# Performance work log

Hardware: AMD Instinct MI355X
Metric: run time of the kernel (lower is better)

The kernel has to match this reference:

```python
import jax, jax.numpy as jnp
import numpy as np

OBS_DIM = 512
ACT_DIM = 32
HIDDEN_DIM = 1024
MSG_DIM = 128
POS_EM_DIM = 128
T = 256


def pos_table(n, dim):
    pos = np.arange(n)[:, None].astype(np.float64)
    j = np.arange(dim)[None, :]
    tab = pos / np.power(10000.0, 2 * (j // 2) / dim)
    tab[:, 0::2] = np.sin(tab[:, 0::2])
    tab[:, 1::2] = np.cos(tab[:, 1::2])
    return tab.astype(np.float32)


def setup_inputs() -> dict:
    key = jax.random.key(0)
    ks = jax.random.split(key, 12)
    in_dim = 1 + ACT_DIM
    s = 0.1
    return {
        "obs": jax.random.normal(ks[0], (T, OBS_DIM), jnp.float32),
        "prev_act": jax.random.normal(ks[1], (T, ACT_DIM), jnp.float32),
        "in_shift": jnp.zeros((OBS_DIM,), jnp.float32),
        "in_scale": jnp.ones((OBS_DIM,), jnp.float32),
        "pos_embedding": jnp.asarray(pos_table(HIDDEN_DIM, POS_EM_DIM)),
        "W_ih": s * jax.random.normal(ks[2], (4 * POS_EM_DIM, in_dim), jnp.float32),
        "b_ih": s * jax.random.normal(ks[3], (4 * POS_EM_DIM,), jnp.float32),
        "W_hh": s * jax.random.normal(ks[4], (4 * POS_EM_DIM, POS_EM_DIM), jnp.float32),
        "b_hh": s * jax.random.normal(ks[5], (4 * POS_EM_DIM,), jnp.float32),
        "Wq": s * jax.random.normal(ks[6], (MSG_DIM, POS_EM_DIM), jnp.float32),
        "bq": s * jax.random.normal(ks[7], (MSG_DIM,), jnp.float32),
        "Wk": s * jax.random.normal(ks[8], (MSG_DIM, POS_EM_DIM), jnp.float32),
        "bk": s * jax.random.normal(ks[9], (MSG_DIM,), jnp.float32),
    }


def reference(obs, prev_act, in_shift, in_scale, pos_embedding,
              W_ih, b_ih, W_hh, b_hh, Wq, bq, Wk, bk):
    # input normalization (buffers default to identity)
    x = (obs - in_shift) / (in_scale + 1e-8)  # (T, obs_dim)
    # query projection of the positional table is constant across steps
    q = pos_embedding @ Wq.T + bq             # (hidden_dim, msg_dim)
    inv_scale = 1.0 / jnp.sqrt(jnp.float32(MSG_DIM))

    def step(carry, inp):
        h, c = carry                            # (obs_dim, pos_em_dim) each
        s, a = inp                              # (obs_dim,), (act_dim,)
        # state-action pair: each obs scalar paired with the full prev action
        xa = jnp.concatenate(
            [s[:, None], jnp.broadcast_to(a, (OBS_DIM, ACT_DIM))], axis=-1)
        gates = xa @ W_ih.T + b_ih + h @ W_hh.T + b_hh
        i, f, g, o = jnp.split(gates, 4, axis=-1)  # torch LSTMCell gate order
        c = jax.nn.sigmoid(f) * c + jax.nn.sigmoid(i) * jnp.tanh(g)
        h = jax.nn.sigmoid(o) * jnp.tanh(c)
        k = h @ Wk.T + bk                       # (obs_dim, msg_dim)
        w = jnp.tanh((q @ k.T) * inv_scale)     # (hidden_dim, obs_dim)
        out = w @ s                             # (hidden_dim,)
        return (h, c), out

    h0 = jnp.zeros((OBS_DIM, POS_EM_DIM), x.dtype)
    c0 = jnp.zeros_like(h0)
    _, outs = jax.lax.scan(step, (h0, c0), (x, prev_act))
    return jnp.tanh(outs)                       # (T, hidden_dim)
```

## Files before the change

kernel.cpp:

```cpp
#include <hip/hip_runtime.h>
#include <hip/hip_fp16.h>

#define T_STEPS 256
#define OBS 512
#define ACT 32
#define HID 1024
#define PED 128
#define MSG 128
#define GATES 512
#define HSTR 136
#define KSTR 17
#define L1 1.4426950408889634f
#define L2C 2.8853900817779268f
#define QSCALE 0.2550348805576823f

typedef _Float16 half8  __attribute__((ext_vector_type(8)));
typedef float    floatx4 __attribute__((ext_vector_type(4)));

__device__ __forceinline__ float fast_exp2(float x) { return __builtin_amdgcn_exp2f(x); }
__device__ __forceinline__ float fast_rcp(float x)  { return __builtin_amdgcn_rcpf(x); }
__device__ __forceinline__ float tanh_f(float x) {
    return fmaf(-2.0f, fast_rcp(fast_exp2(2.8853900817779268f * x) + 1.0f), 1.0f);
}

__global__ void k_pre(const float* __restrict__ obs, const float* __restrict__ act,
                      const float* __restrict__ shift, const float* __restrict__ scale,
                      const float* __restrict__ W_ih, const float* __restrict__ b_ih,
                      const float* __restrict__ b_hh,
                      float* __restrict__ xnorm, float* __restrict__ apre_p) {
    int t = blockIdx.x;
    int tid = threadIdx.x;
    __shared__ float a_s[ACT];
    if (tid < ACT) a_s[tid] = act[t * ACT + tid];
    __syncthreads();
    for (int n = tid; n < OBS; n += 256) {
        xnorm[t * OBS + n] = (obs[t * OBS + n] - shift[n]) / (scale[n] + 1e-8f);
    }
    for (int j = tid; j < GATES; j += 256) {
        float acc = b_ih[j] + b_hh[j];
        const float* wr = W_ih + j * 33 + 1;
#pragma unroll
        for (int u = 0; u < ACT; ++u) acc = fmaf(a_s[u], wr[u], acc);
        int g = j >> 7, p = j & 127;
        apre_p[t * GATES + p * 4 + g] = acc;
    }
}

__global__ void k_qproj(const float* __restrict__ pe, const float* __restrict__ Wq,
                        const float* __restrict__ bq, const float* __restrict__ Wk,
                        const float* __restrict__ bk,
                        _Float16* __restrict__ qh, float* __restrict__ cb) {
    int m = blockIdx.x;
    int d = threadIdx.x;
    __shared__ float pe_s[PED];
    __shared__ float q_s[PED];
    __shared__ float red_s[2];
    pe_s[d] = pe[m * PED + d];
    __syncthreads();
    const float* wr = Wq + d * PED;
    float a = bq[d];
#pragma unroll 8
    for (int p = 0; p < PED; ++p) a = fmaf(pe_s[p], wr[p], a);
    q_s[d] = a;
    float pb = a * bk[d];
#pragma unroll
    for (int off = 32; off; off >>= 1) pb += __shfl_xor(pb, off, 64);
    if ((d & 63) == 0) red_s[d >> 6] = pb;
    __syncthreads();
    float acc = 0.f;
#pragma unroll 8
    for (int p = 0; p < PED; ++p) acc = fmaf(q_s[p], Wk[p * PED + d], acc);
    qh[m * PED + d] = (_Float16)(acc * QSCALE);
    if (d == 0) cb[m] = (red_s[0] + red_s[1]) * QSCALE;
}

__global__ __launch_bounds__(512, 1)
void k_lstm(const float* __restrict__ xnorm, const float* __restrict__ apre_p,
            const float* __restrict__ W_ih, const float* __restrict__ W_hh,
            _Float16* __restrict__ H16) {
    const int tid = threadIdx.x;
    const int lane = tid & 63, wv = tid >> 6;
    const int l15 = lane & 15, quad = lane >> 4;
    const int n0 = blockIdx.x * 8;
    const int p = 16 * wv + l15;
    const int base = (quad & 1) * 4 + ((quad >> 1) * 2);

    half8 bfr[4][4];
    float wih0[4];
#pragma unroll
    for (int g = 0; g < 4; ++g) {
        const int col = 128 * g + p;
        const float* wrow = W_hh + (size_t)col * PED;
#pragma unroll
        for (int c = 0; c < 4; ++c) {
            const int k0 = c * 32 + quad * 8;
            float4 f0 = *(const float4*)(wrow + k0);
            float4 f1 = *(const float4*)(wrow + k0 + 4);
            bfr[g][c] = (half8){(_Float16)f0.x, (_Float16)f0.y, (_Float16)f0.z, (_Float16)f0.w,
                                (_Float16)f1.x, (_Float16)f1.y, (_Float16)f1.z, (_Float16)f1.w};
        }
        wih0[g] = W_ih[(size_t)col * 33];
    }

    __shared__ _Float16 h_s[2][16 * HSTR];
    __shared__ float x_s[T_STEPS * 8];

    for (int idx = tid; idx < T_STEPS * 8; idx += 512)
        x_s[idx] = xnorm[(idx >> 3) * OBS + n0 + (idx & 7)];
    for (int idx = tid; idx < 2 * 16 * HSTR; idx += 512)
        ((_Float16*)h_s)[idx] = (_Float16)0.f;

    float c0 = 0.f, c1 = 0.f;
    const float* apl = apre_p + p * 4;
    float4 ap = *(const float4*)(apl);
    __syncthreads();

    int buf = 0;
    for (int t = 0; t < T_STEPS; ++t) {
        half8 af[4];
        const _Float16* hb = h_s[buf] + l15 * HSTR + quad * 8;
#pragma unroll
        for (int c = 0; c < 4; ++c) af[c] = *(const half8*)(hb + c * 32);

        floatx4 acc[4];
#pragma unroll
        for (int g = 0; g < 4; ++g) {
            acc[g] = (floatx4){0.f, 0.f, 0.f, 0.f};
#pragma unroll
            for (int c = 0; c < 4; ++c)
                acc[g] = __builtin_amdgcn_mfma_f32_16x16x32_f16(
                    af[c], bfr[g][c], acc[g], 0, 0, 0);
        }

        const int tn = (t + 1 < T_STEPS) ? t + 1 : t;
        float4 ap_n = *(const float4*)(apl + tn * GATES);

        float gA[4], gB[4];
#pragma unroll
        for (int g = 0; g < 4; ++g) {
            float s2 = __shfl_xor(acc[g][2], 32, 64);
            float s3 = __shfl_xor(acc[g][3], 32, 64);
            gA[g] = (quad < 2) ? acc[g][0] : s2;
            gB[g] = (quad < 2) ? acc[g][1] : s3;
        }

        const float xA = x_s[t * 8 + base];
        const float xB = x_s[t * 8 + base + 1];
        float gi0 = fmaf(xA, wih0[0], gA[0] + ap.x);
        float gf0 = fmaf(xA, wih0[1], gA[1] + ap.y);
        float gg0 = fmaf(xA, wih0[2], gA[2] + ap.z);
        float go0 = fmaf(xA, wih0[3], gA[3] + ap.w);
        float gi1 = fmaf(xB, wih0[0], gB[0] + ap.x);
        float gf1 = fmaf(xB, wih0[1], gB[1] + ap.y);
        float gg1 = fmaf(xB, wih0[2], gB[2] + ap.z);
        float go1 = fmaf(xB, wih0[3], gB[3] + ap.w);

        float Di0 = 1.f + fast_exp2(fminf(-L1 * gi0, 20.f));
        float Df0 = 1.f + fast_exp2(fminf(-L1 * gf0, 20.f));
        float Dg0 = 1.f + fast_exp2(fminf(L2C * gg0, 20.f));
        float Di1 = 1.f + fast_exp2(fminf(-L1 * gi1, 20.f));
        float Df1 = 1.f + fast_exp2(fminf(-L1 * gf1, 20.f));
        float Dg1 = 1.f + fast_exp2(fminf(L2C * gg1, 20.f));
        float t0 = Df0 * Dg0, C0 = Di0 * t0;
        float t1 = Df1 * Dg1, C1 = Di1 * t1;
        float rp = fast_rcp(C0 * C1);
        float rA = rp * C1, rB = rp * C0;
        float iDi0 = rA * t0, iDf0 = rA * (Di0 * Dg0), iDg0 = rA * (Di0 * Df0);
        float iDi1 = rB * t1, iDf1 = rB * (Di1 * Dg1), iDg1 = rB * (Di1 * Df1);
        float cn0 = fmaf(iDf0, c0, iDi0 * fmaf(-2.f, iDg0, 1.f));
        float cn1 = fmaf(iDf1, c1, iDi1 * fmaf(-2.f, iDg1, 1.f));
        c0 = cn0; c1 = cn1;
        float Do0 = 1.f + fast_exp2(fminf(-L1 * go0, 20.f));
        float Do1 = 1.f + fast_exp2(fminf(-L1 * go1, 20.f));
        float Dc0 = 1.f + fast_exp2(fminf(L2C * cn0, 20.f));
        float Dc1 = 1.f + fast_exp2(fminf(L2C * cn1, 20.f));
        float m0 = Do0 * Dc0, m1 = Do1 * Dc1;
        float rq = fast_rcp(m0 * m1);
        float qA = rq * m1, qB = rq * m0;
        float iDo0 = qA * Dc0, iDc0 = qA * Do0;
        float iDo1 = qB * Dc1, iDc1 = qB * Do1;
        _Float16 hA = (_Float16)(iDo0 * fmaf(-2.f, iDc0, 1.f));
        _Float16 hB = (_Float16)(iDo1 * fmaf(-2.f, iDc1, 1.f));

        _Float16* hn = h_s[buf ^ 1];
        hn[base * HSTR + p] = hA;
        hn[(base + 1) * HSTR + p] = hB;
        _Float16* Hg = H16 + (size_t)t * (OBS * MSG) + (size_t)(n0 + base) * MSG + p;
        Hg[0] = hA;
        Hg[MSG] = hB;

        ap = ap_n;
        buf ^= 1;
        __syncthreads();
    }
}

__global__ __launch_bounds__(256, 4)
void k_attn(const _Float16* __restrict__ qh, const float* __restrict__ cb,
            const _Float16* __restrict__ H16, const float* __restrict__ xnorm,
            float* __restrict__ outp) {
    const int t = blockIdx.x >> 3;
    const int mq = blockIdx.x & 7;
    const int tid = threadIdx.x;
    const int lane = tid & 63, wave = tid >> 6;
    const int l15 = lane & 15, quad = lane >> 4;
    const int m0 = mq * 128 + wave * 32;

    half8 afrag[2][4];
    floatx4 cbv[2];
#pragma unroll
    for (int mt = 0; mt < 2; ++mt) {
        const half8* qrow = (const half8*)(qh + (size_t)(m0 + mt * 16 + l15) * PED);
#pragma unroll
        for (int c = 0; c < 4; ++c) afrag[mt][c] = qrow[c * 4 + quad];
        cbv[mt] = *(const floatx4*)(cb + m0 + mt * 16 + quad * 4);
    }

    __shared__ half8 kbuf[64 * KSTR];
    __shared__ float s_s[64];

    float outacc[8];
#pragma unroll
    for (int i = 0; i < 8; ++i) outacc[i] = 0.f;

    const half8* Ht = (const half8*)(H16 + (size_t)t * (OBS * MSG));
    half8 pf[4];
    float sf = 0.f;
#pragma unroll
    for (int i = 0; i < 4; ++i) pf[i] = Ht[i * 256 + tid];
    if (tid < 64) sf = xnorm[t * OBS + tid];

    for (int ch = 0; ch < 8; ++ch) {
        __syncthreads();
#pragma unroll
        for (int i = 0; i < 4; ++i) {
            int f = i * 256 + tid;
            kbuf[(f >> 4) * KSTR + (f & 15)] = pf[i];
        }
        if (tid < 64) s_s[tid] = sf;
        __syncthreads();
        if (ch < 7) {
            const half8* Hn = Ht + (ch + 1) * 1024;
#pragma unroll
            for (int i = 0; i < 4; ++i) pf[i] = Hn[i * 256 + tid];
            if (tid < 64) sf = xnorm[t * OBS + (ch + 1) * 64 + tid];
        }

#pragma unroll
        for (int nt = 0; nt < 4; ++nt) {
            half8 bfrag[4];
#pragma unroll
            for (int c = 0; c < 4; ++c)
                bfrag[c] = kbuf[(nt * 16 + l15) * KSTR + c * 4 + quad];

            floatx4 acc[2];
#pragma unroll
            for (int mt = 0; mt < 2; ++mt) {
                acc[mt] = cbv[mt];
#pragma unroll
                for (int c = 0; c < 4; ++c)
                    acc[mt] = __builtin_amdgcn_mfma_f32_16x16x32_f16(
                        afrag[mt][c], bfrag[c], acc[mt], 0, 0, 0);
            }

            const float sv = s_s[nt * 16 + l15];
#pragma unroll
            for (int mt = 0; mt < 2; ++mt) {
                float E0 = fast_exp2(fminf(acc[mt][0], 20.f));
                float E1 = fast_exp2(fminf(acc[mt][1], 20.f));
                float E2 = fast_exp2(fminf(acc[mt][2], 20.f));
                float E3 = fast_exp2(fminf(acc[mt][3], 20.f));
                float D0 = 1.f + E0, D1 = 1.f + E1, D2 = 1.f + E2, D3 = 1.f + E3;
                float m01 = D0 * D1, m23 = D2 * D3;
                float rp = fast_rcp(m01 * m23);
                float rA = rp * m23, rB = rp * m01;
                float i0 = rA * D1, i1 = rA * D0, i2 = rB * D3, i3 = rB * D2;
                outacc[mt * 4 + 0] = fmaf(fmaf(-2.f, i0, 1.f), sv, outacc[mt * 4 + 0]);
                outacc[mt * 4 + 1] = fmaf(fmaf(-2.f, i1, 1.f), sv, outacc[mt * 4 + 1]);
                outacc[mt * 4 + 2] = fmaf(fmaf(-2.f, i2, 1.f), sv, outacc[mt * 4 + 2]);
                outacc[mt * 4 + 3] = fmaf(fmaf(-2.f, i3, 1.f), sv, outacc[mt * 4 + 3]);
            }
        }
    }

#pragma unroll
    for (int i = 0; i < 8; ++i) {
        float v = outacc[i];
        v += __shfl_xor(v, 1, 16);
        v += __shfl_xor(v, 2, 16);
        v += __shfl_xor(v, 4, 16);
        v += __shfl_xor(v, 8, 16);
        outacc[i] = v;
    }
    if (l15 == 0) {
        const int mbase = m0 + quad * 4;
#pragma unroll
        for (int mt = 0; mt < 2; ++mt)
#pragma unroll
            for (int r = 0; r < 4; ++r)
                outp[(size_t)t * HID + mbase + mt * 16 + r] = tanh_f(outacc[mt * 4 + r]);
    }
}

extern "C" void kernel_launch(void* const* d_in, const int* in_sizes, int n_in,
                              void* d_out, int out_size, void* d_ws, size_t ws_size,
                              hipStream_t stream) {
    const float* obs      = (const float*)d_in[0];
    const float* prev_act = (const float*)d_in[1];
    const float* in_shift = (const float*)d_in[2];
    const float* in_scale = (const float*)d_in[3];
    const float* pos_emb  = (const float*)d_in[4];
    const float* W_ih     = (const float*)d_in[5];
    const float* b_ih     = (const float*)d_in[6];
    const float* W_hh     = (const float*)d_in[7];
    const float* b_hh     = (const float*)d_in[8];
    const float* Wq       = (const float*)d_in[9];
    const float* bq       = (const float*)d_in[10];
    const float* Wk       = (const float*)d_in[11];
    const float* bk       = (const float*)d_in[12];
    float* outp = (float*)d_out;

    float* ws = (float*)d_ws;
    float* xnorm  = ws;
    float* apre_p = ws + 131072;
    _Float16* qh  = (_Float16*)(ws + 262144);
    float* cbuf   = ws + 327680;
    _Float16* H16 = (_Float16*)(ws + 328704);

    k_pre<<<T_STEPS, 256, 0, stream>>>(obs, prev_act, in_shift, in_scale,
                                       W_ih, b_ih, b_hh, xnorm, apre_p);
    k_qproj<<<HID, 128, 0, stream>>>(pos_emb, Wq, bq, Wk, bk, qh, cbuf);
    k_lstm<<<64, 512, 0, stream>>>(xnorm, apre_p, W_ih, W_hh, H16);
    k_attn<<<T_STEPS * 8, 256, 0, stream>>>(qh, cbuf, H16, xnorm, outp);
}
```

Before: 335.2 us.

## Halve LSTM rows per block, seed MFMA with bias, stream attention K directly

The LSTM kernel now handles 4 obs rows per block instead of 8 and launches 128 blocks. This spreads the serial recurrence over more CUs and removes the cross-lane shuffles and the two-row gate math, while leaving more MFMA rows padded. The gate bias is loaded into the MFMA accumulator as its starting value. The attention kernel drops its LDS staging and barriers and loads H fragments from global memory into registers with a one-tile prefetch, trading shared-memory reuse for fewer syncs.

```diff
diff --git a/kernel.cpp b/kernel.cpp
--- a/kernel.cpp
+++ b/kernel.cpp
@@ -9,7 +9,6 @@
 #define MSG 128
 #define GATES 512
 #define HSTR 136
-#define KSTR 17
 #define L1 1.4426950408889634f
 #define L2C 2.8853900817779268f
 #define QSCALE 0.2550348805576823f
@@ -81,9 +80,8 @@
     const int tid = threadIdx.x;
     const int lane = tid & 63, wv = tid >> 6;
     const int l15 = lane & 15, quad = lane >> 4;
-    const int n0 = blockIdx.x * 8;
+    const int n0 = blockIdx.x * 4;
     const int p = 16 * wv + l15;
-    const int base = (quad & 1) * 4 + ((quad >> 1) * 2);
 
     half8 bfr[4][4];
     float wih0[4];
@@ -103,18 +101,19 @@
     }
 
     __shared__ _Float16 h_s[2][16 * HSTR];
-    __shared__ float x_s[T_STEPS * 8];
-
-    for (int idx = tid; idx < T_STEPS * 8; idx += 512)
-        x_s[idx] = xnorm[(idx >> 3) * OBS + n0 + (idx & 7)];
+    __shared__ float x_s[T_STEPS * 4];
+
+    for (int idx = tid; idx < T_STEPS * 4; idx += 512)
+        x_s[idx] = xnorm[(idx >> 2) * OBS + n0 + (idx & 3)];
     for (int idx = tid; idx < 2 * 16 * HSTR; idx += 512)
         ((_Float16*)h_s)[idx] = (_Float16)0.f;
 
-    float c0 = 0.f, c1 = 0.f;
+    float c0 = 0.f;
     const float* apl = apre_p + p * 4;
     float4 ap = *(const float4*)(apl);
     __syncthreads();
 
+    _Float16* Hg = H16 + (size_t)(n0 + quad) * MSG + p;
     int buf = 0;
     for (int t = 0; t < T_STEPS; ++t) {
         half8 af[4];
@@ -123,71 +122,43 @@
         for (int c = 0; c < 4; ++c) af[c] = *(const half8*)(hb + c * 32);
 
         floatx4 acc[4];
-#pragma unroll
-        for (int g = 0; g < 4; ++g) {
-            acc[g] = (floatx4){0.f, 0.f, 0.f, 0.f};
+        acc[0] = (floatx4){ap.x, ap.x, ap.x, ap.x};
+        acc[1] = (floatx4){ap.y, ap.y, ap.y, ap.y};
+        acc[2] = (floatx4){ap.z, ap.z, ap.z, ap.z};
+        acc[3] = (floatx4){ap.w, ap.w, ap.w, ap.w};
+#pragma unroll
+        for (int g = 0; g < 4; ++g)
 #pragma unroll
             for (int c = 0; c < 4; ++c)
                 acc[g] = __builtin_amdgcn_mfma_f32_16x16x32_f16(
                     af[c], bfr[g][c], acc[g], 0, 0, 0);
-        }
 
         const int tn = (t + 1 < T_STEPS) ? t + 1 : t;
         float4 ap_n = *(const float4*)(apl + tn * GATES);
 
-        float gA[4], gB[4];
-#pragma unroll
-        for (int g = 0; g < 4; ++g) {
-            float s2 = __shfl_xor(acc[g][2], 32, 64);
-            float s3 = __shfl_xor(acc[g][3], 32, 64);
-            gA[g] = (quad < 2) ? acc[g][0] : s2;
-            gB[g] = (quad < 2) ? acc[g][1] : s3;
-        }
-
-        const float xA = x_s[t * 8 + base];
-        const float xB = x_s[t * 8 + base + 1];
-        float gi0 = fmaf(xA, wih0[0], gA[0] + ap.x);
-        float gf0 = fmaf(xA, wih0[1], gA[1] + ap.y);
-        float gg0 = fmaf(xA, wih0[2], gA[2] + ap.z);
-        float go0 = fmaf(xA, wih0[3], gA[3] + ap.w);
-        float gi1 = fmaf(xB, wih0[0], gB[0] + ap.x);
-        float gf1 = fmaf(xB, wih0[1], gB[1] + ap.y);
-        float gg1 = fmaf(xB, wih0[2], gB[2] + ap.z);
-        float go1 = fmaf(xB, wih0[3], gB[3] + ap.w);
-
-        float Di0 = 1.f + fast_exp2(fminf(-L1 * gi0, 20.f));
-        float Df0 = 1.f + fast_exp2(fminf(-L1 * gf0, 20.f));
-        float Dg0 = 1.f + fast_exp2(fminf(L2C * gg0, 20.f));
-        float Di1 = 1.f + fast_exp2(fminf(-L1 * gi1, 20.f));
-        float Df1 = 1.f + fast_exp2(fminf(-L1 * gf1, 20.f));
-        float Dg1 = 1.f + fast_exp2(fminf(L2C * gg1, 20.f));
-        float t0 = Df0 * Dg0, C0 = Di0 * t0;
-        float t1 = Df1 * Dg1, C1 = Di1 * t1;
-        float rp = fast_rcp(C0 * C1);
-        float rA = rp * C1, rB = rp * C0;
-        float iDi0 = rA * t0, iDf0 = rA * (Di0 * Dg0), iDg0 = rA * (Di0 * Df0);
-        float iDi1 = rB * t1, iDf1 = rB * (Di1 * Dg1), iDg1 = rB * (Di1 * Df1);
-        float cn0 = fmaf(iDf0, c0, iDi0 * fmaf(-2.f, iDg0, 1.f));
-        float cn1 = fmaf(iDf1, c1, iDi1 * fmaf(-2.f, iDg1, 1.f));
-        c0 = cn0; c1 = cn1;
-        float Do0 = 1.f + fast_exp2(fminf(-L1 * go0, 20.f));
-        float Do1 = 1.f + fast_exp2(fminf(-L1 * go1, 20.f));
-        float Dc0 = 1.f + fast_exp2(fminf(L2C * cn0, 20.f));
-        float Dc1 = 1.f + fast_exp2(fminf(L2C * cn1, 20.f));
-        float m0 = Do0 * Dc0, m1 = Do1 * Dc1;
-        float rq = fast_rcp(m0 * m1);
-        float qA = rq * m1, qB = rq * m0;
-        float iDo0 = qA * Dc0, iDc0 = qA * Do0;
-        float iDo1 = qB * Dc1, iDc1 = qB * Do1;
-        _Float16 hA = (_Float16)(iDo0 * fmaf(-2.f, iDc0, 1.f));
-        _Float16 hB = (_Float16)(iDo1 * fmaf(-2.f, iDc1, 1.f));
-
-        _Float16* hn = h_s[buf ^ 1];
-        hn[base * HSTR + p] = hA;
-        hn[(base + 1) * HSTR + p] = hB;
-        _Float16* Hg = H16 + (size_t)t * (OBS * MSG) + (size_t)(n0 + base) * MSG + p;
-        Hg[0] = hA;
-        Hg[MSG] = hB;
+        const float x = x_s[t * 4 + quad];
+        float gi = fmaf(x, wih0[0], acc[0][0]);
+        float gf = fmaf(x, wih0[1], acc[1][0]);
+        float gg = fmaf(x, wih0[2], acc[2][0]);
+        float go = fmaf(x, wih0[3], acc[3][0]);
+
+        float Di = 1.f + fast_exp2(fminf(-L1 * gi, 20.f));
+        float Df = 1.f + fast_exp2(fminf(-L1 * gf, 20.f));
+        float Dg = 1.f + fast_exp2(fminf(L2C * gg, 20.f));
+        float DfDg = Df * Dg, DiDg = Di * Dg, DiDf = Di * Df;
+        float r3 = fast_rcp(Di * DfDg);
+        float iDi = r3 * DfDg, iDf = r3 * DiDg, iDg = r3 * DiDf;
+        float cn = fmaf(iDf, c0, iDi * fmaf(-2.f, iDg, 1.f));
+        c0 = cn;
+        float Do = 1.f + fast_exp2(fminf(-L1 * go, 20.f));
+        float Dc = 1.f + fast_exp2(fminf(L2C * cn, 20.f));
+        float r2 = fast_rcp(Do * Dc);
+        float iDo = r2 * Dc, iDc = r2 * Do;
+        _Float16 hq = (_Float16)(iDo * fmaf(-2.f, iDc, 1.f));
+
+        h_s[buf ^ 1][(4 * quad) * HSTR + p] = hq;
+        Hg[0] = hq;
+        Hg += OBS * MSG;
 
         ap = ap_n;
         buf ^= 1;
@@ -216,71 +187,59 @@
         cbv[mt] = *(const floatx4*)(cb + m0 + mt * 16 + quad * 4);
     }
 
-    __shared__ half8 kbuf[64 * KSTR];
-    __shared__ float s_s[64];
-
     float outacc[8];
 #pragma unroll
     for (int i = 0; i < 8; ++i) outacc[i] = 0.f;
 
-    const half8* Ht = (const half8*)(H16 + (size_t)t * (OBS * MSG));
-    half8 pf[4];
-    float sf = 0.f;
-#pragma unroll
-    for (int i = 0; i < 4; ++i) pf[i] = Ht[i * 256 + tid];
-    if (tid < 64) sf = xnorm[t * OBS + tid];
-
-    for (int ch = 0; ch < 8; ++ch) {
-        __syncthreads();
-#pragma unroll
-        for (int i = 0; i < 4; ++i) {
-            int f = i * 256 + tid;
-            kbuf[(f >> 4) * KSTR + (f & 15)] = pf[i];
-        }
-        if (tid < 64) s_s[tid] = sf;
-        __syncthreads();
-        if (ch < 7) {
-            const half8* Hn = Ht + (ch + 1) * 1024;
-#pragma unroll
-            for (int i = 0; i < 4; ++i) pf[i] = Hn[i * 256 + tid];
-            if (tid < 64) sf = xnorm[t * OBS + (ch + 1) * 64 + tid];
-        }
-
-#pragma unroll
-        for (int nt = 0; nt < 4; ++nt) {
-            half8 bfrag[4];
+    const _Float16* Hb = H16 + (size_t)t * (OBS * MSG) + (size_t)l15 * MSG + quad * 8;
+    const float* xb = xnorm + t * OBS + l15;
+
+    half8 bf[4];
+    float sv;
+#pragma unroll
+    for (int c = 0; c < 4; ++c) bf[c] = *(const half8*)(Hb + c * 32);
+    sv = xb[0];
+
+    for (int nt = 0; nt < 32; ++nt) {
+        half8 bfn[4];
+        float svn = 0.f;
+        if (nt < 31) {
+            const _Float16* Hn = Hb + (nt + 1) * (16 * MSG);
+#pragma unroll
+            for (int c = 0; c < 4; ++c) bfn[c] = *(const half8*)(Hn + c * 32);
+            svn = xb[(nt + 1) * 16];
+        }
+
+        floatx4 acc[2];
+#pragma unroll
+        for (int mt = 0; mt < 2; ++mt) {
+            acc[mt] = cbv[mt];
 #pragma unroll
             for (int c = 0; c < 4; ++c)
-                bfrag[c] = kbuf[(nt * 16 + l15) * KSTR + c * 4 + quad];
-
-            floatx4 acc[2];
-#pragma unroll
-            for (int mt = 0; mt < 2; ++mt) {
-                acc[mt] = cbv[mt];
-#pragma unroll
-                for (int c = 0; c < 4; ++c)
-                    acc[mt] = __builtin_amdgcn_mfma_f32_16x16x32_f16(
-                        afrag[mt][c], bfrag[c], acc[mt], 0, 0, 0);
-            }
-
-            const float sv = s_s[nt * 16 + l15];
-#pragma unroll
-            for (int mt = 0; mt < 2; ++mt) {
-                float E0 = fast_exp2(fminf(acc[mt][0], 20.f));
-                float E1 = fast_exp2(fminf(acc[mt][1], 20.f));
-                float E2 = fast_exp2(fminf(acc[mt][2], 20.f));
-                float E3 = fast_exp2(fminf(acc[mt][3], 20.f));
-                float D0 = 1.f + E0, D1 = 1.f + E1, D2 = 1.f + E2, D3 = 1.f + E3;
-                float m01 = D0 * D1, m23 = D2 * D3;
-                float rp = fast_rcp(m01 * m23);
-                float rA = rp * m23, rB = rp * m01;
-                float i0 = rA * D1, i1 = rA * D0, i2 = rB * D3, i3 = rB * D2;
-                outacc[mt * 4 + 0] = fmaf(fmaf(-2.f, i0, 1.f), sv, outacc[mt * 4 + 0]);
-                outacc[mt * 4 + 1] = fmaf(fmaf(-2.f, i1, 1.f), sv, outacc[mt * 4 + 1]);
-                outacc[mt * 4 + 2] = fmaf(fmaf(-2.f, i2, 1.f), sv, outacc[mt * 4 + 2]);
-                outacc[mt * 4 + 3] = fmaf(fmaf(-2.f, i3, 1.f), sv, outacc[mt * 4 + 3]);
-            }
-        }
+                acc[mt] = __builtin_amdgcn_mfma_f32_16x16x32_f16(
+                    afrag[mt][c], bf[c], acc[mt], 0, 0, 0);
+        }
+
+#pragma unroll
+        for (int mt = 0; mt < 2; ++mt) {
+            float E0 = fast_exp2(fminf(acc[mt][0], 20.f));
+            float E1 = fast_exp2(fminf(acc[mt][1], 20.f));
+            float E2 = fast_exp2(fminf(acc[mt][2], 20.f));
+            float E3 = fast_exp2(fminf(acc[mt][3], 20.f));
+            float D0 = 1.f + E0, D1 = 1.f + E1, D2 = 1.f + E2, D3 = 1.f + E3;
+            float m01 = D0 * D1, m23 = D2 * D3;
+            float rp = fast_rcp(m01 * m23);
+            float rA = rp * m23, rB = rp * m01;
+            float i0 = rA * D1, i1 = rA * D0, i2 = rB * D3, i3 = rB * D2;
+            outacc[mt * 4 + 0] = fmaf(fmaf(-2.f, i0, 1.f), sv, outacc[mt * 4 + 0]);
+            outacc[mt * 4 + 1] = fmaf(fmaf(-2.f, i1, 1.f), sv, outacc[mt * 4 + 1]);
+            outacc[mt * 4 + 2] = fmaf(fmaf(-2.f, i2, 1.f), sv, outacc[mt * 4 + 2]);
+            outacc[mt * 4 + 3] = fmaf(fmaf(-2.f, i3, 1.f), sv, outacc[mt * 4 + 3]);
+        }
+
+#pragma unroll
+        for (int c = 0; c < 4; ++c) bf[c] = bfn[c];
+        sv = svn;
     }
 
 #pragma unroll
@@ -330,6 +289,6 @@
     k_pre<<<T_STEPS, 256, 0, stream>>>(obs, prev_act, in_shift, in_scale,
                                        W_ih, b_ih, b_hh, xnorm, apre_p);
     k_qproj<<<HID, 128, 0, stream>>>(pos_emb, Wq, bq, Wk, bk, qh, cbuf);
-    k_lstm<<<64, 512, 0, stream>>>(xnorm, apre_p, W_ih, W_hh, H16);
+    k_lstm<<<128, 512, 0, stream>>>(xnorm, apre_p, W_ih, W_hh, H16);
     k_attn<<<T_STEPS * 8, 256, 0, stream>>>(qh, cbuf, H16, xnorm, outp);
 }
```

New measurement: 365.8 us. +9.1%, slower.
